# Kernel tuning notes

Measured on AMD Instinct MI355X. Metric: run time of the kernel, lower is better.

The kernel has to match this reference:

```python
import jax, jax.numpy as jnp
import numpy as np
import math

# Config (matches init_kwargs / input_specs)
N_ENT = 50000      # number of entities
N_REL = 500        # number of relations
HID = 64           # args.hidden_dim = per-axis dim d; entity dim = 3d, relation dim = 4d
E = 500000         # number of edges
EMB_RANGE = 1.0    # embedding_range
PI = 3.1415926235897933


def setup_inputs() -> dict:
    key = jax.random.key(0)
    k1, k2, k3, k4, k5 = jax.random.split(key, 5)
    entities = jax.random.normal(k1, (N_ENT, 3 * HID), dtype=jnp.float32)
    relations = jax.random.normal(k2, (N_REL, 4 * HID), dtype=jnp.float32)
    head = jax.random.randint(k3, (E,), 0, N_ENT, dtype=jnp.int32)
    rel = jax.random.randint(k4, (E,), 0, N_REL, dtype=jnp.int32)
    tail = jax.random.randint(k5, (E,), 0, N_ENT, dtype=jnp.int32)
    edge_index = jnp.stack([head, rel, tail], axis=0)  # (3, E)
    return {"entities": entities, "relations": relations, "edge_index": edge_index}


def do_trans(ent, rel):
    """Rot3DE rotation: rotate 3D entity point (per feature dim) by the
    quaternion encoded in rel = (axis_x, axis_y, axis_z, theta). is_head_rel=True branch.
    ent: (E, 3d), rel: (E, 4d) -> (E, 4d)"""
    ex, ey, ez = jnp.split(ent, 3, axis=-1)            # each (E, d)
    rx, ry, rz, theta = jnp.split(rel, 4, axis=-1)     # each (E, d)
    theta = theta / (EMB_RANGE / PI)
    sin = jnp.sin(theta)
    w = jnp.cos(theta)
    # F.normalize(stack([sin*rx, sin*ry, sin*rz]), dim=0): unit rotation axis (sign of sin folded in)
    t = jnp.stack([sin * rx, sin * ry, sin * rz], axis=0)  # (3, E, d)
    norm = jnp.sqrt(jnp.sum(t * t, axis=0, keepdims=True))
    n = t / jnp.maximum(norm, 1e-12)
    # quaternion q = (w, u) with u = |sin(theta)| * unit_axis  (sin sign already in n)
    s = jnp.sqrt(jnp.clip(1.0 - w * w, 0.0, None))
    ux, uy, uz = s * n[0], s * n[1], s * n[2]
    # Hamilton product q (x) p with pure quaternion p = (0, ex, ey, ez)  [head direction]
    x_score = w * ex + (uy * ez - uz * ey)
    y_score = w * ey + (uz * ex - ux * ez)
    z_score = w * ez + (ux * ey - uy * ex)
    w_score = -(ux * ex + uy * ey + uz * ez)
    return jnp.concatenate([x_score, y_score, z_score, w_score], axis=-1)  # (E, 4d)


def reference(entities, relations, edge_index):
    head, rel_id, tail = edge_index[0], edge_index[1], edge_index[2]
    # eff_do_trans's unique-based dedup is a pure compute optimization; the
    # math is identical to the direct per-edge transform below.
    qv = do_trans(entities[head], relations[rel_id])  # (E, 4d) keys/values
    # GAT_update: key = [gathered tail entity (3d) ; zeros(d)]
    k = jnp.concatenate(
        [entities[tail], jnp.zeros((E, HID), dtype=entities.dtype)], axis=-1
    )  # (E, 4d)
    embed_dim = 4 * HID
    alpha = jnp.sum(k * qv, axis=-1) / math.sqrt(embed_dim)  # (E,)
    # scatter_softmax over destination nodes (stable segment softmax)
    m = jax.ops.segment_max(alpha, tail, num_segments=N_ENT)
    m = jnp.where(jnp.isfinite(m), m, 0.0)  # empty segments
    e = jnp.exp(alpha - m[tail])
    denom = jax.ops.segment_sum(e, tail, num_segments=N_ENT)
    attn = e / denom[tail]  # (E,)
    # weighted scatter_add -> (N_ENT, 4d)
    out = jax.ops.segment_sum(qv * attn[:, None], tail, num_segments=N_ENT)
    return out
```

## Files before the change

### kernel.cpp

```cpp
#include <hip/hip_runtime.h>
#include <stdint.h>
#include <math.h>

#define HID 64
#define PI_F 3.14159262235897933f

typedef float v2f __attribute__((ext_vector_type(2)));

__device__ __forceinline__ unsigned short f2bf(float f) {
    unsigned u = __float_as_uint(f);
    return (unsigned short)((u + 0x7FFFu + ((u >> 16) & 1u)) >> 16);
}
__device__ __forceinline__ float bflo(unsigned v) { return __uint_as_float(v << 16); }
__device__ __forceinline__ float bfhi(unsigned v) { return __uint_as_float(v & 0xFFFF0000u); }

__global__ void prep(const float* __restrict__ rel, uint2* __restrict__ quat16, int nrel,
                     const int* __restrict__ eidx, int E, int* __restrict__ hist,
                     const float* __restrict__ ent, uint4* __restrict__ ent16, int nconv,
                     int qblocks, int eblocks) {
    const int b = blockIdx.x;
    if (b < qblocks) {
        int i = b * 256 + threadIdx.x;
        if (i >= nrel * HID) return;
        int r = i >> 6, j = i & 63;
        const float* base = rel + (size_t)r * 4 * HID;
        float rx = base[j];
        float ry = base[HID + j];
        float rz = base[2 * HID + j];
        float th = base[3 * HID + j];
        float theta = th * PI_F;
        float sn = sinf(theta);
        float w  = cosf(theta);
        float tx = sn * rx, ty = sn * ry, tz = sn * rz;
        float norm = sqrtf(tx * tx + ty * ty + tz * tz);
        float inv = 1.0f / fmaxf(norm, 1e-12f);
        float s = sqrtf(fmaxf(1.0f - w * w, 0.0f));
        float ux = s * tx * inv, uy = s * ty * inv, uz = s * tz * inv;
        quat16[i] = make_uint2(((unsigned)f2bf(ux) << 16) | f2bf(w),
                               ((unsigned)f2bf(uz) << 16) | f2bf(uy));
    } else if (b < qblocks + eblocks) {
        int e = (b - qblocks) * 256 + threadIdx.x;
        if (e >= E) return;
        atomicAdd(hist + eidx[2 * E + e], 1);
    } else {
        int u = (b - qblocks - eblocks) * 256 + threadIdx.x;
        if (u >= nconv) return;
        const float4* src = (const float4*)ent + 2 * (size_t)u;
        float4 a = src[0], c = src[1];
        ent16[u] = make_uint4(((unsigned)f2bf(a.y) << 16) | f2bf(a.x),
                              ((unsigned)f2bf(a.w) << 16) | f2bf(a.z),
                              ((unsigned)f2bf(c.y) << 16) | f2bf(c.x),
                              ((unsigned)f2bf(c.w) << 16) | f2bf(c.z));
    }
}

__global__ void scan1(const int* __restrict__ hist, int* __restrict__ base,
                      int* __restrict__ partial, int n) {
    __shared__ int buf[256];
    int tid = threadIdx.x;
    int gid = blockIdx.x * 256 + tid;
    int v = (gid < n) ? hist[gid] : 0;
    buf[tid] = v;
    __syncthreads();
    #pragma unroll
    for (int off = 1; off < 256; off <<= 1) {
        int x = (tid >= off) ? buf[tid - off] : 0;
        __syncthreads();
        buf[tid] += x;
        __syncthreads();
    }
    if (gid < n) base[gid] = buf[tid] - v;
    if (tid == 255) partial[blockIdx.x] = buf[255];
}

__global__ void scan23(int* __restrict__ base, int* __restrict__ base2,
                       const int* __restrict__ partial,
                       int nb, int n, int E) {
    __shared__ int buf[256];
    int tid = threadIdx.x;
    int v = (tid < nb) ? partial[tid] : 0;
    buf[tid] = v;
    __syncthreads();
    #pragma unroll
    for (int off = 1; off < 256; off <<= 1) {
        int x = (tid >= off) ? buf[tid - off] : 0;
        __syncthreads();
        buf[tid] += x;
        __syncthreads();
    }
    int bsum = ((int)blockIdx.x < nb) ? partial[blockIdx.x] : 0;
    int boff = buf[blockIdx.x] - bsum;
    int gid = blockIdx.x * 256 + tid;
    if (gid < n) {
        int bv = base[gid] + boff;
        base[gid] = bv;
        base2[gid] = bv;
    } else if (gid == n) {
        base[n] = E;
    }
}

__global__ void scatter_hr(const int* __restrict__ eidx, int E,
                           int* __restrict__ base2,
                           unsigned* __restrict__ hrp) {
    int e = blockIdx.x * blockDim.x + threadIdx.x;
    if (e >= E) return;
    int t = eidx[2 * E + e];
    int pos = atomicAdd(base2 + t, 1);
    hrp[pos] = ((unsigned)eidx[e] << 9) | (unsigned)eidx[E + e];
}

__global__ void __launch_bounds__(256)
seg_reduce(const unsigned* __restrict__ ent32,
           const uint4* __restrict__ quat4,
           const unsigned* __restrict__ hrp,
           const int* __restrict__ base,
           int n_ent,
           float* __restrict__ out) {
    const int lane = threadIdx.x & 63;
    const int half = lane >> 5;
    const int j    = lane & 31;
    const int wid = (blockIdx.x * blockDim.x + threadIdx.x) >> 6;
    const int nw  = (gridDim.x * blockDim.x) >> 6;

    for (int t = wid; t < n_ent; t += nw) {
        int start = base[t];
        int end   = base[t + 1];
        float2* o2 = (float2*)(out + (size_t)t * (4 * HID));
        const int ob0 = half * 64 + j;
        const int ob1 = ob0 + 32;
        if (start == end) {
            o2[ob0] = make_float2(0.f, 0.f);
            o2[ob1] = make_float2(0.f, 0.f);
            continue;
        }
        int last = end - 1;

        const unsigned* kb = ent32 + (size_t)t * 96;
        unsigned ku0 = kb[j], ku1 = kb[32 + j], ku2 = kb[64 + j];
        v2f kx = {bflo(ku0), bfhi(ku0)};
        v2f ky = {bflo(ku1), bfhi(ku1)};
        v2f kz = {bflo(ku2), bfhi(ku2)};

        float dnm = 0.0f;
        v2f fx = {0.f, 0.f}, fy = fx, fz = fx, fw = fx;

        for (int kk = start; kk < end; kk += 2) {
            int e = kk + half;
            bool valid = (e < end);
            unsigned her = hrp[min(e, last)];
            unsigned hidx = her >> 9;
            unsigned ridx = her & 511u;

            const unsigned* hb = ent32 + (size_t)hidx * 96;
            unsigned u0 = hb[j], u1 = hb[32 + j], u2 = hb[64 + j];
            uint4 qa = quat4[ridx * 32 + j];

            v2f ex = {bflo(u0), bfhi(u0)};
            v2f ey = {bflo(u1), bfhi(u1)};
            v2f ez = {bflo(u2), bfhi(u2)};
            v2f w  = {bflo(qa.x), bflo(qa.z)};
            v2f ux = {bfhi(qa.x), bfhi(qa.z)};
            v2f uy = {bflo(qa.y), bflo(qa.w)};
            v2f uz = {bfhi(qa.y), bfhi(qa.w)};

            v2f rqx = w * ex + uy * ez - uz * ey;
            v2f rqy = w * ey + uz * ex - ux * ez;
            v2f rqz = w * ez + ux * ey - uy * ex;
            v2f rqw = -(ux * ex + uy * ey + uz * ez);

            v2f p2 = kx * rqx + ky * rqy + kz * rqz;
            float p = p2.x + p2.y;
            p += __shfl_xor(p, 1, 64);
            p += __shfl_xor(p, 2, 64);
            p += __shfl_xor(p, 4, 64);
            p += __shfl_xor(p, 8, 64);
            p += __shfl_xor(p, 16, 64);

            float pe = valid ? __expf(p * 0.0625f) : 0.0f;
            v2f pe2 = {pe, pe};
            dnm += pe;
            fx += pe2 * rqx;
            fy += pe2 * rqy;
            fz += pe2 * rqz;
            fw += pe2 * rqw;
        }

        dnm += __shfl_xor(dnm, 32, 64);
        fx.x += __shfl_xor(fx.x, 32, 64); fx.y += __shfl_xor(fx.y, 32, 64);
        fy.x += __shfl_xor(fy.x, 32, 64); fy.y += __shfl_xor(fy.y, 32, 64);
        fz.x += __shfl_xor(fz.x, 32, 64); fz.y += __shfl_xor(fz.y, 32, 64);
        fw.x += __shfl_xor(fw.x, 32, 64); fw.y += __shfl_xor(fw.y, 32, 64);

        float inv = (dnm > 0.0f) ? 1.0f / dnm : 0.0f;
        v2f s0 = half ? fz : fx;
        v2f s1 = half ? fw : fy;
        o2[ob0] = make_float2(s0.x * inv, s0.y * inv);
        o2[ob1] = make_float2(s1.x * inv, s1.y * inv);
    }
}

extern "C" void kernel_launch(void* const* d_in, const int* in_sizes, int n_in,
                              void* d_out, int out_size, void* d_ws, size_t ws_size,
                              hipStream_t stream) {
    const float* ent  = (const float*)d_in[0];
    const float* rel  = (const float*)d_in[1];
    const int*   eidx = (const int*)d_in[2];
    float* out = (float*)d_out;

    const int n_ent = in_sizes[0] / (3 * HID);
    const int n_rel = in_sizes[1] / (4 * HID);
    const int E     = in_sizes[2] / 3;

    uint8_t* wp = (uint8_t*)d_ws;
    unsigned* hrp = (unsigned*)wp;                   wp += (size_t)E * 4;
    int*  hist    = (int*)wp;                        wp += (size_t)n_ent * 4;
    int*  base    = (int*)wp;                        wp += (size_t)(n_ent + 1) * 4;
    int*  base2   = (int*)wp;                        wp += (size_t)n_ent * 4;
    int*  partial = (int*)wp;                        wp += 256 * 4;
    wp = (uint8_t*)(((uintptr_t)wp + 15) & ~(uintptr_t)15);
    uint2* quat16 = (uint2*)wp;                      wp += (size_t)n_rel * HID * sizeof(uint2);
    wp = (uint8_t*)(((uintptr_t)wp + 15) & ~(uintptr_t)15);
    uint4* ent16  = (uint4*)wp;                      wp += (size_t)n_ent * 3 * HID * 2;
    (void)ws_size;

    hipMemsetAsync(hist, 0, (size_t)n_ent * 4, stream);

    const int qblocks = (n_rel * HID + 255) / 256;
    const int eblocks = (E + 255) / 256;
    const int nconv   = n_ent * 3 * HID / 8;
    const int cblocks = (nconv + 255) / 256;
    prep<<<qblocks + eblocks + cblocks, 256, 0, stream>>>(
        rel, quat16, n_rel, eidx, E, hist, ent, ent16, nconv, qblocks, eblocks);

    const int nb = (n_ent + 255) / 256;
    scan1<<<nb, 256, 0, stream>>>(hist, base, partial, n_ent);
    scan23<<<(n_ent + 1 + 255) / 256, 256, 0, stream>>>(base, base2, partial, nb, n_ent, E);

    scatter_hr<<<eblocks, 256, 0, stream>>>(eidx, E, base2, hrp);

    seg_reduce<<<2048, 256, 0, stream>>>((const unsigned*)ent16, (const uint4*)quat16,
                                         hrp, base, n_ent, out);
}
```

Baseline: 123.5 us.

## Fold block-offset scan into scatter and reduce kernels; use nontemporal stores

Drops the separate scan23 launch. The scatter kernel and the segment-reduce kernel each redo the small partial-sum prefix scan in shared memory and add the block offset on the fly, with a separate zeroed cursor array taking the place of base2. Nontemporal stores and loads are used for the bf16 entity conversion, the output writes and the edge-list reads, to reduce cache pollution. The trade-off is one fewer launch against redundant per-block scans in 2048 reduce blocks and roughly 2000 scatter blocks.

Result: slower. 134.0 us (+8.5%).

```diff
diff --git a/kernel.cpp b/kernel.cpp
--- a/kernel.cpp
+++ b/kernel.cpp
@@ -47,10 +47,15 @@
         if (u >= nconv) return;
         const float4* src = (const float4*)ent + 2 * (size_t)u;
         float4 a = src[0], c = src[1];
-        ent16[u] = make_uint4(((unsigned)f2bf(a.y) << 16) | f2bf(a.x),
-                              ((unsigned)f2bf(a.w) << 16) | f2bf(a.z),
-                              ((unsigned)f2bf(c.y) << 16) | f2bf(c.x),
-                              ((unsigned)f2bf(c.w) << 16) | f2bf(c.z));
+        unsigned p0 = ((unsigned)f2bf(a.y) << 16) | f2bf(a.x);
+        unsigned p1 = ((unsigned)f2bf(a.w) << 16) | f2bf(a.z);
+        unsigned p2 = ((unsigned)f2bf(c.y) << 16) | f2bf(c.x);
+        unsigned p3 = ((unsigned)f2bf(c.w) << 16) | f2bf(c.z);
+        unsigned* dst = (unsigned*)(ent16 + u);
+        __builtin_nontemporal_store(p0, dst + 0);
+        __builtin_nontemporal_store(p1, dst + 1);
+        __builtin_nontemporal_store(p2, dst + 2);
+        __builtin_nontemporal_store(p3, dst + 3);
     }
 }
 
@@ -73,11 +78,13 @@
     if (tid == 255) partial[blockIdx.x] = buf[255];
 }
 
-__global__ void scan23(int* __restrict__ base, int* __restrict__ base2,
-                       const int* __restrict__ partial,
-                       int nb, int n, int E) {
+__global__ void scatter_hr(const int* __restrict__ eidx, int E,
+                           const int* __restrict__ base,
+                           const int* __restrict__ partial, int nb,
+                           int* __restrict__ cursor,
+                           unsigned* __restrict__ hrp) {
     __shared__ int buf[256];
-    int tid = threadIdx.x;
+    const int tid = threadIdx.x;
     int v = (tid < nb) ? partial[tid] : 0;
     buf[tid] = v;
     __syncthreads();
@@ -88,25 +95,15 @@
         buf[tid] += x;
         __syncthreads();
     }
-    int bsum = ((int)blockIdx.x < nb) ? partial[blockIdx.x] : 0;
-    int boff = buf[blockIdx.x] - bsum;
-    int gid = blockIdx.x * 256 + tid;
-    if (gid < n) {
-        int bv = base[gid] + boff;
-        base[gid] = bv;
-        base2[gid] = bv;
-    } else if (gid == n) {
-        base[n] = E;
-    }
-}
-
-__global__ void scatter_hr(const int* __restrict__ eidx, int E,
-                           int* __restrict__ base2,
-                           unsigned* __restrict__ hrp) {
-    int e = blockIdx.x * blockDim.x + threadIdx.x;
+    int ex = buf[tid] - v;
+    __syncthreads();
+    buf[tid] = ex;
+    __syncthreads();
+
+    int e = blockIdx.x * 256 + tid;
     if (e >= E) return;
     int t = eidx[2 * E + e];
-    int pos = atomicAdd(base2 + t, 1);
+    int pos = base[t] + buf[t >> 8] + atomicAdd(cursor + t, 1);
     hrp[pos] = ((unsigned)eidx[e] << 9) | (unsigned)eidx[E + e];
 }
 
@@ -115,8 +112,28 @@
            const uint4* __restrict__ quat4,
            const unsigned* __restrict__ hrp,
            const int* __restrict__ base,
-           int n_ent,
+           const int* __restrict__ partial, int nb,
+           int n_ent, int E,
            float* __restrict__ out) {
+    __shared__ int buf[256];
+    {
+        const int tid = threadIdx.x;
+        int v = (tid < nb) ? partial[tid] : 0;
+        buf[tid] = v;
+        __syncthreads();
+        #pragma unroll
+        for (int off = 1; off < 256; off <<= 1) {
+            int x = (tid >= off) ? buf[tid - off] : 0;
+            __syncthreads();
+            buf[tid] += x;
+            __syncthreads();
+        }
+        int ex = buf[tid] - v;
+        __syncthreads();
+        buf[tid] = ex;
+        __syncthreads();
+    }
+
     const int lane = threadIdx.x & 63;
     const int half = lane >> 5;
     const int j    = lane & 31;
@@ -124,14 +141,15 @@
     const int nw  = (gridDim.x * blockDim.x) >> 6;
 
     for (int t = wid; t < n_ent; t += nw) {
-        int start = base[t];
-        int end   = base[t + 1];
-        float2* o2 = (float2*)(out + (size_t)t * (4 * HID));
+        int start = base[t] + buf[t >> 8];
+        int end   = (t + 1 < n_ent) ? (base[t + 1] + buf[(t + 1) >> 8]) : E;
+        v2f* o2 = (v2f*)(out + (size_t)t * (4 * HID));
         const int ob0 = half * 64 + j;
         const int ob1 = ob0 + 32;
         if (start == end) {
-            o2[ob0] = make_float2(0.f, 0.f);
-            o2[ob1] = make_float2(0.f, 0.f);
+            v2f z = {0.f, 0.f};
+            __builtin_nontemporal_store(z, o2 + ob0);
+            __builtin_nontemporal_store(z, o2 + ob1);
             continue;
         }
         int last = end - 1;
@@ -148,7 +166,7 @@
         for (int kk = start; kk < end; kk += 2) {
             int e = kk + half;
             bool valid = (e < end);
-            unsigned her = hrp[min(e, last)];
+            unsigned her = __builtin_nontemporal_load(hrp + min(e, last));
             unsigned hidx = her >> 9;
             unsigned ridx = her & 511u;
 
@@ -195,8 +213,10 @@
         float inv = (dnm > 0.0f) ? 1.0f / dnm : 0.0f;
         v2f s0 = half ? fz : fx;
         v2f s1 = half ? fw : fy;
-        o2[ob0] = make_float2(s0.x * inv, s0.y * inv);
-        o2[ob1] = make_float2(s1.x * inv, s1.y * inv);
+        v2f r0 = {s0.x * inv, s0.y * inv};
+        v2f r1 = {s1.x * inv, s1.y * inv};
+        __builtin_nontemporal_store(r0, o2 + ob0);
+        __builtin_nontemporal_store(r1, o2 + ob1);
     }
 }
 
@@ -215,8 +235,8 @@
     uint8_t* wp = (uint8_t*)d_ws;
     unsigned* hrp = (unsigned*)wp;                   wp += (size_t)E * 4;
     int*  hist    = (int*)wp;                        wp += (size_t)n_ent * 4;
-    int*  base    = (int*)wp;                        wp += (size_t)(n_ent + 1) * 4;
-    int*  base2   = (int*)wp;                        wp += (size_t)n_ent * 4;
+    int*  cursor  = (int*)wp;                        wp += (size_t)n_ent * 4;
+    int*  base    = (int*)wp;                        wp += (size_t)n_ent * 4;
     int*  partial = (int*)wp;                        wp += 256 * 4;
     wp = (uint8_t*)(((uintptr_t)wp + 15) & ~(uintptr_t)15);
     uint2* quat16 = (uint2*)wp;                      wp += (size_t)n_rel * HID * sizeof(uint2);
@@ -224,7 +244,7 @@
     uint4* ent16  = (uint4*)wp;                      wp += (size_t)n_ent * 3 * HID * 2;
     (void)ws_size;
 
-    hipMemsetAsync(hist, 0, (size_t)n_ent * 4, stream);
+    hipMemsetAsync(hist, 0, (size_t)n_ent * 8, stream);
 
     const int qblocks = (n_rel * HID + 255) / 256;
     const int eblocks = (E + 255) / 256;
@@ -235,10 +255,9 @@
 
     const int nb = (n_ent + 255) / 256;
     scan1<<<nb, 256, 0, stream>>>(hist, base, partial, n_ent);
-    scan23<<<(n_ent + 1 + 255) / 256, 256, 0, stream>>>(base, base2, partial, nb, n_ent, E);
-
-    scatter_hr<<<eblocks, 256, 0, stream>>>(eidx, E, base2, hrp);
+
+    scatter_hr<<<eblocks, 256, 0, stream>>>(eidx, E, base, partial, nb, cursor, hrp);
 
     seg_reduce<<<2048, 256, 0, stream>>>((const unsigned*)ent16, (const uint4*)quat16,
-                                         hrp, base, n_ent, out);
-}
+                                         hrp, base, partial, nb, n_ent, E, out);
+}
```
